# Kernel tuning notes

Measured on AMD Instinct MI355X. Metric: run time of the kernel, lower is better.

The kernel has to match this reference:

```python
import jax, jax.numpy as jnp
import numpy as np

B = 65536; D1 = 64; D2 = 64; DC = 128; K = 8; DFF = 1024
NPP = 3 * K - 1                      # 23 params per output dim (non-adaptive)
MIN_BIN = 0.1; MIN_DERIV = 1e-3; ALPHA = 2.0
DEFAULT = 3.0; DL = -DEFAULT; DD = 2 * DEFAULT; MIN_DELTA = MIN_BIN * K
SHIFT = float(np.log(np.e - 1.0))
SHIFT_DX = float(np.log(np.exp(DD - MIN_DELTA) - 1.0))
EPS = 1e-6


def setup_inputs() -> dict:
    key = jax.random.key(0)
    ks = jax.random.split(key, 8)
    x1 = jax.random.normal(ks[0], (B, D1), dtype=jnp.float32)
    x2 = jax.random.normal(ks[1], (B, D2), dtype=jnp.float32)
    context = jax.random.normal(ks[2], (B, DC), dtype=jnp.float32)
    mask1 = jnp.ones((B, D1), dtype=jnp.float32)
    din = 2 * D1 + DC
    W0 = jax.random.normal(ks[3], (din, DFF), dtype=jnp.float32) / np.sqrt(din)
    b0 = jnp.zeros((DFF,), jnp.float32)
    W1 = jax.random.normal(ks[4], (DFF, DFF), dtype=jnp.float32) / np.sqrt(DFF)
    b1 = jnp.zeros((DFF,), jnp.float32)
    W2 = jax.random.normal(ks[5], (DFF, DFF), dtype=jnp.float32) / np.sqrt(DFF)
    b2 = jnp.zeros((DFF,), jnp.float32)
    W3 = jax.random.normal(ks[6], (DFF, NPP * D2), dtype=jnp.float32) / np.sqrt(DFF)
    b3 = jnp.zeros((NPP * D2,), jnp.float32)
    return dict(x1=x1, x2=x2, context=context, mask1=mask1,
                W0=W0, b0=b0, W1=W1, b1=b1, W2=W2, b2=b2, W3=W3, b3=b3)


def _rq_forward(x1, x2, context, mask1, W0, b0, W1, b1, W2, b2, W3, b3):
    # --- conditioner MLP: input = concat(x1, mask1, context) ---
    h = jnp.concatenate([x1, mask1, context], axis=-1)
    h = jax.nn.relu(h @ W0 + b0)
    h = jax.nn.relu(h @ W1 + b1)
    h = jax.nn.relu(h @ W2 + b2)
    params = (h @ W3 + b3).reshape(x1.shape[0], D2, NPP)  # [B, D2, 23]

    w_raw = params[..., :K]
    h_raw = params[..., K:2 * K]
    d_raw = params[..., 2 * K:3 * K - 1]
    zeros = jnp.zeros(params.shape[:-1] + (1,), params.dtype)  # non-adaptive raw params

    # --- _constrain ---
    log_weight = ALPHA * jnp.tanh(zeros / ALPHA)          # -> 0
    weight = jnp.exp(log_weight)                          # -> 1
    bias = ALPHA * jnp.tanh(zeros / ALPHA)                # -> 0
    derivs = MIN_DERIV + jax.nn.softplus(d_raw + SHIFT)
    derivs = jnp.concatenate([weight, derivs, weight], axis=-1)  # [B, D2, K+1]
    left = DL + DD * jnp.tanh(zeros / DD)                 # -> -3
    delta_x = MIN_DELTA + jax.nn.softplus(zeros + SHIFT_DX)
    right = left + delta_x                                # -> +3
    bottom = weight * left + bias
    top = weight * right + bias

    w = jax.nn.softmax(w_raw, axis=-1)
    w = MIN_BIN + (1.0 - MIN_BIN * K) * w
    cw = jnp.pad(jnp.cumsum(w, axis=-1), ((0, 0), (0, 0), (1, 0)))
    cw = (right - left) * cw + left                       # cumwidths [B, D2, K+1]
    hh = jax.nn.softmax(h_raw, axis=-1)
    hh = MIN_BIN + (1.0 - MIN_BIN * K) * hh
    ch = jnp.pad(jnp.cumsum(hh, axis=-1), ((0, 0), (0, 0), (1, 0)))
    ch = (top - bottom) * ch + bottom                     # cumheights [B, D2, K+1]

    widths = cw[..., 1:] - cw[..., :-1]
    heights = ch[..., 1:] - ch[..., :-1]

    # --- bin search (searchsorted right=True on bumped cumwidths) ---
    bumped = jnp.concatenate([cw[..., :-1], cw[..., -1:] + EPS], axis=-1)
    idx = jnp.clip(jnp.sum(bumped <= x2[..., None], axis=-1) - 1, 0, K - 1)[..., None]

    gat = lambda t: jnp.take_along_axis(t, idx, axis=-1)[..., 0]
    x_k = gat(cw); x_kd = gat(widths)
    y_k = gat(ch); y_kd = gat(heights)
    s_k = gat(heights / widths)
    d0 = gat(derivs); d1 = gat(derivs[..., 1:])

    # --- forward rational-quadratic spline ---
    xi = (x2 - x_k) / x_kd
    xi1m = xi * (1.0 - xi)
    alpha_k = y_kd * (s_k * xi ** 2 + d0 * xi1m)
    beta_k = s_k + (d1 + d0 - 2.0 * s_k) * xi1m
    z_sp = y_k + alpha_k / jnp.maximum(beta_k, 1e-8)
    num = s_k ** 2 * (d1 * xi ** 2 + 2.0 * s_k * xi1m + d0 * (1.0 - xi) ** 2)
    ld_sp = jnp.log(jnp.maximum(num, 1e-8)) - 2.0 * jnp.log(jnp.maximum(beta_k, 1e-8))

    # --- affine tails ---
    lw = log_weight[..., 0]; bs = bias[..., 0]
    z_af = jnp.exp(lw) * x2 + bs
    ld_af = jnp.broadcast_to(lw, x2.shape)

    l2 = jnp.broadcast_to(left[..., 0], x2.shape)
    r2 = jnp.broadcast_to(right[..., 0], x2.shape)
    inside = (l2 <= x2) & (x2 < r2)
    z2 = jnp.where(inside, z_sp, z_af)
    ld = jnp.where(inside, ld_sp, ld_af)
    return z2, ld.sum(-1)


def reference(x1, x2, context, mask1, W0, b0, W1, b1, W2, b2, W3, b3):
    return _rq_forward(x1, x2, context, mask1, W0, b0, W1, b1, W2, b2, W3, b3)
```

## Files before the change

### kernel.cpp

```cpp
#include <hip/hip_runtime.h>


typedef __bf16 bf16_t;
typedef __bf16 bf16x8 __attribute__((ext_vector_type(8)));
typedef float f32x4 __attribute__((ext_vector_type(4)));

#define GLOAD_LDS16(g, l)                                               \
  __builtin_amdgcn_global_load_lds(                                     \
      (const __attribute__((address_space(1))) void*)(g),               \
      (__attribute__((address_space(3))) void*)(l), 16, 0, 0)

#define WAITVM(N) asm volatile("s_waitcnt vmcnt(" #N ")" ::: "memory")
#define SBAR() __builtin_amdgcn_s_barrier()

__device__ __forceinline__ void xcd_remap(int& bx, int& by) {
  const int gx = gridDim.x;
  const int nwg = gx * gridDim.y;
  const int id = blockIdx.y * gx + blockIdx.x;
  const int nid = (id & 7) * (nwg >> 3) + (id >> 3);
  bx = nid % gx;
  by = nid / gx;
}

__global__ __launch_bounds__(256) void transpose_w(
    const float* __restrict__ W, bf16_t* __restrict__ Wt,
    int K, int N, int Npad) {
  __shared__ float tile[64][65];
  const int kt = blockIdx.x * 64;
  const int nt = blockIdx.y * 64;
  const int r4 = threadIdx.x >> 6;
  const int c = threadIdx.x & 63;
#pragma unroll
  for (int i = 0; i < 16; i++) {
    int r = i * 4 + r4;
    int gn = nt + c;
    tile[r][c] = (gn < N) ? W[(size_t)(kt + r) * N + gn] : 0.0f;
  }
  __syncthreads();
#pragma unroll
  for (int i = 0; i < 16; i++) {
    int r = i * 4 + r4;
    Wt[(size_t)(nt + r) * K + kt + c] = (bf16_t)tile[c][r];
  }
}

__global__ __launch_bounds__(256) void transpose_w3p(
    const float* __restrict__ W3, bf16_t* __restrict__ Wt) {
  __shared__ float tile[64][65];
  const int kt = blockIdx.x * 64;
  const int nt = blockIdx.y * 64;
  const int r4 = threadIdx.x >> 6;
  const int c = threadIdx.x & 63;
  const int np = nt + c;
  const int d = np / 24, p = np % 24;
#pragma unroll
  for (int i = 0; i < 16; i++) {
    int r = i * 4 + r4;
    tile[r][c] = (p < 23) ? W3[(size_t)(kt + r) * 1472 + d * 23 + p] : 0.0f;
  }
  __syncthreads();
#pragma unroll
  for (int i = 0; i < 16; i++) {
    int r = i * 4 + r4;
    Wt[(size_t)(nt + r) * 1024 + kt + c] = (bf16_t)tile[c][r];
  }
}

__global__ __launch_bounds__(256) void prep_b3(const float* __restrict__ b3,
                                               float* __restrict__ b3p) {
  int t = blockIdx.x * 256 + threadIdx.x;
  if (t < 1536) {
    int d = t / 24, p = t % 24;
    b3p[t] = (p < 23) ? b3[d * 23 + p] : 0.0f;
  }
}

__global__ __launch_bounds__(256) void build_x(
    const float* __restrict__ x1, const float* __restrict__ mask1,
    const float* __restrict__ ctx, bf16_t* __restrict__ X,
    float* __restrict__ ld_out, int boff) {
  int idx = blockIdx.x * 256 + threadIdx.x;
  int bl = idx >> 8;
  int c = idx & 255;
  size_t b = (size_t)(boff + bl);
  float v;
  if (c < 64)       v = x1[b * 64 + c];
  else if (c < 128) v = mask1[b * 64 + (c - 64)];
  else              v = ctx[b * 128 + (c - 128)];
  X[(size_t)bl * 256 + c] = (bf16_t)v;
  if (c == 0) ld_out[b] = 0.0f;
}

__global__ __launch_bounds__(512, 2) void gemm_bt(
    const bf16_t* __restrict__ A, const bf16_t* __restrict__ Bt,
    const float* __restrict__ bias, bf16_t* __restrict__ Cout, int N, int K) {
  __shared__ __align__(16) bf16_t sm[65536];
  const int tid = threadIdx.x;
  const int lane = tid & 63;
  const int w = tid >> 6;
  int bx, by;
  xcd_remap(bx, by);
  const int m0 = by * 256;
  const int n0 = bx * 256;
  const int wmi = w >> 2;
  const int wnj = w & 3;
  const int lrow = lane & 15;
  const int quad = lane >> 4;

  const int byteoff = tid * 16;
  const int srow = byteoff >> 6;
  const int sqs = ((byteoff >> 4) & 3) ^ ((srow >> 1) & 3);
  const bf16_t* gA0 = A + (size_t)(m0 + srow) * K + sqs * 8;
  const bf16_t* gA1 = A + (size_t)(m0 + 128 + srow) * K + sqs * 8;
  const bf16_t* gB0 = Bt + (size_t)(n0 + srow) * K + sqs * 8;
  const bf16_t* gB1 = Bt + (size_t)(n0 + 128 + srow) * K + sqs * 8;
  const int dstT = tid * 8;

#define ST_A(PTR, D, RH)                                                 \
  do {                                                                   \
    GLOAD_LDS16(PTR, sm + (D) * 16384 + (RH) * 8192 + dstT);             \
    GLOAD_LDS16(PTR + 32, sm + (D) * 16384 + (RH) * 8192 + 4096 + dstT); \
    PTR += 64;                                                           \
  } while (0)
#define ST_B(PTR, D, CH)                                                 \
  do {                                                                   \
    GLOAD_LDS16(PTR, sm + 32768 + (D) * 16384 + (CH) * 8192 + dstT);     \
    GLOAD_LDS16(PTR + 32,                                                \
                sm + 32768 + (D) * 16384 + (CH) * 8192 + 4096 + dstT);   \
    PTR += 64;                                                           \
  } while (0)

  int aoff[8];
#pragma unroll
  for (int mi = 0; mi < 8; mi++) {
    const int r = mi * 16 + lrow;
    aoff[mi] = wmi * 8192 + r * 32 + (quad ^ ((r >> 1) & 3)) * 8;
  }
  int boff[4];
#pragma unroll
  for (int nj = 0; nj < 4; nj++) {
    const int c = (wnj & 1) * 64 + nj * 16 + lrow;
    boff[nj] = 32768 + (wnj >> 1) * 8192 + c * 32 + (quad ^ ((c >> 1) & 3)) * 8;
  }

#define RD_AF(DST, D, MIB)                                               \
  _Pragma("unroll") for (int q = 0; q < 4; q++)                          \
    _Pragma("unroll") for (int kk = 0; kk < 2; kk++)                     \
      DST[q][kk] =                                                       \
          *(const bf16x8*)(sm + (D) * 16384 + kk * 4096 + aoff[(MIB) + q]);
#define RD_BF(DST, D, NJB)                                               \
  _Pragma("unroll") for (int q = 0; q < 2; q++)                          \
    _Pragma("unroll") for (int kk = 0; kk < 2; kk++)                     \
      DST[q][kk] =                                                       \
          *(const bf16x8*)(sm + (D) * 16384 + kk * 4096 + boff[(NJB) + q]);
#define MM(AF, BF, MIB, NJB)                                             \
  __builtin_amdgcn_s_setprio(1);                                         \
  _Pragma("unroll") for (int q = 0; q < 4; q++)                          \
    _Pragma("unroll") for (int p = 0; p < 2; p++)                        \
      _Pragma("unroll") for (int kk = 0; kk < 2; kk++)                   \
        acc[(MIB) + q][(NJB) + p] = __builtin_amdgcn_mfma_f32_16x16x32_bf16( \
            AF[q][kk], BF[p][kk], acc[(MIB) + q][(NJB) + p], 0, 0, 0);   \
  __builtin_amdgcn_s_setprio(0);

  f32x4 acc[8][4];
#pragma unroll
  for (int i = 0; i < 8; i++)
#pragma unroll
    for (int j = 0; j < 4; j++) acc[i][j] = (f32x4){0.f, 0.f, 0.f, 0.f};

  ST_A(gA0, 0, 0);
  ST_A(gA1, 0, 1);
  ST_B(gB0, 0, 0);
  ST_B(gB1, 0, 1);
  ST_A(gA0, 1, 0);
  ST_A(gA1, 1, 1);

  const int nI = K >> 7;
  for (int i = 0; i < nI; i++) {
    const bool nl = (i + 1 < nI);
    bf16x8 afA[4][2], afB[4][2], bfrA[2][2], bfrB[2][2];
    WAITVM(4);
    SBAR();
    ST_B(gB0, 1, 0);
    RD_AF(afA, 0, 0);
    RD_BF(bfrA, 0, 0);
    MM(afA, bfrA, 0, 0);
    SBAR();
    ST_B(gB1, 1, 1);
    RD_AF(afB, 0, 4);
    MM(afB, bfrA, 4, 0);
    SBAR();
    if (nl) ST_A(gA0, 0, 0);
    RD_BF(bfrB, 0, 2);
    MM(afA, bfrB, 0, 2);
    SBAR();
    if (nl) ST_A(gA1, 0, 1);
    MM(afB, bfrB, 4, 2);
    if (nl) { WAITVM(4); } else { WAITVM(0); }
    SBAR();
    if (nl) ST_B(gB0, 0, 0);
    RD_AF(afA, 1, 0);
    RD_BF(bfrA, 1, 0);
    MM(afA, bfrA, 0, 0);
    SBAR();
    if (nl) ST_B(gB1, 0, 1);
    RD_AF(afB, 1, 4);
    MM(afB, bfrA, 4, 0);
    SBAR();
    if (nl) ST_A(gA0, 1, 0);
    RD_BF(bfrB, 1, 2);
    MM(afA, bfrB, 0, 2);
    SBAR();
    if (nl) ST_A(gA1, 1, 1);
    MM(afB, bfrB, 4, 2);
  }
#undef ST_A
#undef ST_B
#undef RD_AF
#undef RD_BF
#undef MM

  float bv[4];
#pragma unroll
  for (int j = 0; j < 4; j++) bv[j] = bias[n0 + wnj * 64 + j * 16 + lrow];
#pragma unroll
  for (int i = 0; i < 8; i++) {
    int rbase = m0 + wmi * 128 + i * 16 + quad * 4;
#pragma unroll
    for (int j = 0; j < 4; j++) {
      int col = n0 + wnj * 64 + j * 16 + lrow;
#pragma unroll
      for (int r = 0; r < 4; r++) {
        float v = fmaxf(acc[i][j][r] + bv[j], 0.0f);
        Cout[(size_t)(rbase + r) * N + col] = (bf16_t)v;
      }
    }
  }
}

__global__ __launch_bounds__(512, 4) void gemm_rq_fused(
    const bf16_t* __restrict__ A, const bf16_t* __restrict__ Bt,
    const float* __restrict__ b3p, const float* __restrict__ x2,
    float* __restrict__ z_out, float* __restrict__ ld_out,
    int boff, int K) {
  union alignas(16) SM {
    struct { bf16_t As[2][128 * 32]; bf16_t Bs[2][192 * 32]; } s;
    bf16_t Pt[128 * 200];
  };
  __shared__ SM sm;
  const int tid = threadIdx.x;
  const int w = tid >> 6;
  const int lane = tid & 63;
  int bx, by;
  xcd_remap(bx, by);
  const int m0 = by * 128;
  const int n0 = bx * 192;
  const int wm = (w & 1) * 64;
  const int wn = (w >> 1) * 48;
  const int lrow = lane & 15;
  const int quad = lane >> 4;

  bf16_t* const smB = &sm.s.As[0][0];

  const bf16_t* gA;
  {
    const int byteoff = (w << 10) + lane * 16;
    const int row = byteoff >> 6;
    const int qs = ((byteoff >> 4) & 3) ^ ((row >> 1) & 3);
    gA = A + (size_t)(m0 + row) * K + qs * 8;
  }
  const bf16_t* gB0;
  const bf16_t* gB1;
  {
    int byteoff = (w << 10) + lane * 16;
    int row = byteoff >> 6;
    int qs = ((byteoff >> 4) & 3) ^ ((row >> 1) & 3);
    gB0 = Bt + (size_t)(n0 + row) * K + qs * 8;
    const int c1 = (w & 3) + 8;
    byteoff = (c1 << 10) + lane * 16;
    row = byteoff >> 6;
    qs = ((byteoff >> 4) & 3) ^ ((row >> 1) & 3);
    gB1 = Bt + (size_t)(n0 + row) * K + qs * 8;
  }
  bf16_t* const dA0 = smB + w * 512;
  bf16_t* const dB0 = smB + 8192 + w * 512;
  bf16_t* const dB1 = smB + 8192 + ((w & 3) + 8) * 512;

  int offA[4], offB3[3];
#pragma unroll
  for (int i = 0; i < 4; i++) {
    const int rowA = wm + i * 16 + lrow;
    offA[i] = rowA * 32 + (quad ^ ((rowA >> 1) & 3)) * 8;
  }
#pragma unroll
  for (int j = 0; j < 3; j++) {
    const int rowB = wn + j * 16 + lrow;
    offB3[j] = rowB * 32 + (quad ^ ((rowB >> 1) & 3)) * 8;
  }

  f32x4 acc[4][3];
#pragma unroll
  for (int i = 0; i < 4; i++)
#pragma unroll
    for (int j = 0; j < 3; j++) acc[i][j] = (f32x4){0.f, 0.f, 0.f, 0.f};

  const int nPair = K >> 6;
  for (int kp = 0; kp < nPair; kp++) {
    GLOAD_LDS16(gA, dA0);
    GLOAD_LDS16(gA + 32, dA0 + 4096);
    GLOAD_LDS16(gB0, dB0);
    GLOAD_LDS16(gB0 + 32, dB0 + 6144);
    if (w < 4) {
      GLOAD_LDS16(gB1, dB1);
      GLOAD_LDS16(gB1 + 32, dB1 + 6144);
      gB1 += 64;
    }
    gA += 64;
    gB0 += 64;
    __syncthreads();
#pragma unroll
    for (int h = 0; h < 2; h++) {
      bf16x8 af[4], bfr[3];
#pragma unroll
      for (int i = 0; i < 4; i++)
        af[i] = *(const bf16x8*)(smB + h * 4096 + offA[i]);
#pragma unroll
      for (int j = 0; j < 3; j++)
        bfr[j] = *(const bf16x8*)(smB + 8192 + h * 6144 + offB3[j]);
#pragma unroll
      for (int i = 0; i < 4; i++)
#pragma unroll
        for (int j = 0; j < 3; j++)
          acc[i][j] = __builtin_amdgcn_mfma_f32_16x16x32_bf16(
              af[i], bfr[j], acc[i][j], 0, 0, 0);
    }
    __syncthreads();
  }

  float bv[3];
#pragma unroll
  for (int j = 0; j < 3; j++) bv[j] = b3p[n0 + wn + j * 16 + lrow];
#pragma unroll
  for (int i = 0; i < 4; i++) {
    const int rbase = wm + i * 16 + quad * 4;
#pragma unroll
    for (int j = 0; j < 3; j++) {
      const int col = wn + j * 16 + lrow;
#pragma unroll
      for (int r = 0; r < 4; r++)
        sm.Pt[(rbase + r) * 200 + col] = (bf16_t)(acc[i][j][r] + bv[j]);
    }
  }
  __syncthreads();

  const float SHIFT = 0.54132485f;
  const float SHIFT_DX = 5.1944682f;
  const float left = -3.0f;
  const float delta_x = 0.8f + log1pf(expf(SHIFT_DX));
  const float right = left + delta_x;
  const float scale = delta_x;
  const int dloc = tid & 7;
  const int dg = bx * 8 + dloc;

#pragma unroll
  for (int rr = 0; rr < 2; rr++) {
    const int row = (tid >> 3) + rr * 64;
    const bf16_t* pr = sm.Pt + row * 200 + dloc * 24;
    const size_t bg = (size_t)(boff + m0 + row);
    const float x = x2[bg * 64 + dg];

    bf16x8 v0 = *(const bf16x8*)(pr);
    bf16x8 v1 = *(const bf16x8*)(pr + 8);
    bf16x8 v2 = *(const bf16x8*)(pr + 16);
    float pv[24];
#pragma unroll
    for (int j = 0; j < 8; j++) pv[j] = (float)v0[j];
#pragma unroll
    for (int j = 0; j < 8; j++) pv[8 + j] = (float)v1[j];
#pragma unroll
    for (int j = 0; j < 8; j++) pv[16 + j] = (float)v2[j];

    float mw = pv[0];
#pragma unroll
    for (int j = 1; j < 8; j++) mw = fmaxf(mw, pv[j]);
    float ew[8], swv = 0.f;
#pragma unroll
    for (int j = 0; j < 8; j++) { ew[j] = expf(pv[j] - mw); swv += ew[j]; }
    float invw = 1.0f / swv;
    float cw[9];
    cw[0] = left;
    float cum = 0.f;
#pragma unroll
    for (int j = 0; j < 8; j++) {
      cum += 0.1f + 0.2f * ew[j] * invw;
      cw[j + 1] = left + scale * cum;
    }
    float mh = pv[8];
#pragma unroll
    for (int j = 9; j < 16; j++) mh = fmaxf(mh, pv[j]);
    float eh[8], shv = 0.f;
#pragma unroll
    for (int j = 0; j < 8; j++) { eh[j] = expf(pv[8 + j] - mh); shv += eh[j]; }
    float invh = 1.0f / shv;
    float chh[9];
    chh[0] = left;
    float cumh = 0.f;
#pragma unroll
    for (int j = 0; j < 8; j++) {
      cumh += 0.1f + 0.2f * eh[j] * invh;
      chh[j + 1] = left + scale * cumh;
    }
    float dv[9];
    dv[0] = 1.0f;
    dv[8] = 1.0f;
#pragma unroll
    for (int j = 0; j < 7; j++) {
      float v = pv[16 + j] + SHIFT;
      dv[j + 1] = 0.001f + ((v > 20.f) ? v : log1pf(expf(v)));
    }
    int cnt = 0;
#pragma unroll
    for (int j = 0; j < 8; j++) cnt += (cw[j] <= x) ? 1 : 0;
    cnt += ((cw[8] + 1e-6f) <= x) ? 1 : 0;
    int idx = cnt - 1;
    idx = idx < 0 ? 0 : (idx > 7 ? 7 : idx);
    float x_k = cw[0], x_k1 = cw[1], y_k = chh[0], y_k1 = chh[1];
    float d0v = dv[0], d1v = dv[1];
#pragma unroll
    for (int j = 1; j < 8; j++) {
      bool s = (idx == j);
      x_k = s ? cw[j] : x_k;
      x_k1 = s ? cw[j + 1] : x_k1;
      y_k = s ? chh[j] : y_k;
      y_k1 = s ? chh[j + 1] : y_k1;
      d0v = s ? dv[j] : d0v;
      d1v = s ? dv[j + 1] : d1v;
    }
    float x_kd = x_k1 - x_k;
    float y_kd = y_k1 - y_k;
    float s_k = y_kd / x_kd;
    float xi = (x - x_k) / x_kd;
    float xi1m = xi * (1.f - xi);
    float alpha_k = y_kd * (s_k * xi * xi + d0v * xi1m);
    float beta_k = s_k + (d1v + d0v - 2.f * s_k) * xi1m;
    float z_sp = y_k + alpha_k / fmaxf(beta_k, 1e-8f);
    float oxi = 1.f - xi;
    float num = s_k * s_k * (d1v * xi * xi + 2.f * s_k * xi1m + d0v * oxi * oxi);
    float ld_sp = logf(fmaxf(num, 1e-8f)) - 2.f * logf(fmaxf(beta_k, 1e-8f));

    bool inside = (left <= x) && (x < right);
    z_out[bg * 64 + dg] = inside ? z_sp : x;
    float ldv = inside ? ld_sp : 0.f;
    ldv += __shfl_xor(ldv, 1);
    ldv += __shfl_xor(ldv, 2);
    ldv += __shfl_xor(ldv, 4);
    if (dloc == 0) atomicAdd(&ld_out[bg], ldv);
  }
}

extern "C" void kernel_launch(void* const* d_in, const int* in_sizes, int n_in,
                              void* d_out, int out_size, void* d_ws,
                              size_t ws_size, hipStream_t stream) {
  const float* x1 = (const float*)d_in[0];
  const float* x2 = (const float*)d_in[1];
  const float* ctx = (const float*)d_in[2];
  const float* mask1 = (const float*)d_in[3];
  const float* W0 = (const float*)d_in[4];
  const float* b0 = (const float*)d_in[5];
  const float* W1 = (const float*)d_in[6];
  const float* b1 = (const float*)d_in[7];
  const float* W2 = (const float*)d_in[8];
  const float* b2 = (const float*)d_in[9];
  const float* W3 = (const float*)d_in[10];
  const float* b3 = (const float*)d_in[11];
  float* out = (float*)d_out;

  const int B = 65536;
  char* ws = (char*)d_ws;

  bf16_t* Wt0 = (bf16_t*)ws;
  bf16_t* Wt1 = (bf16_t*)(ws + 524288);
  bf16_t* Wt2 = (bf16_t*)(ws + 524288 + 2097152);
  bf16_t* Wt3 = (bf16_t*)(ws + 524288 + 2 * 2097152);
  float* b3p = (float*)(ws + 524288 + 2 * 2097152 + 3145728);
  const size_t wend = 524288 + 2 * 2097152 + 3145728 + 8192;

  int C = 4;
  if (wend + (size_t)B * 4096 <= ws_size) C = 1;
  else if (wend + (size_t)(B / 2) * 4096 <= ws_size) C = 2;
  const int Bc = B / C;
  bf16_t* HA = (bf16_t*)(ws + wend);
  char* R = ws + wend + (size_t)Bc * 2048;
  bf16_t* X = (bf16_t*)R;
  bf16_t* HB = (bf16_t*)R;
  float* ld_out = out + (size_t)B * 64;

  transpose_w<<<dim3(4, 16), 256, 0, stream>>>(W0, Wt0, 256, 1024, 1024);
  transpose_w<<<dim3(16, 16), 256, 0, stream>>>(W1, Wt1, 1024, 1024, 1024);
  transpose_w<<<dim3(16, 16), 256, 0, stream>>>(W2, Wt2, 1024, 1024, 1024);
  transpose_w3p<<<dim3(16, 24), 256, 0, stream>>>(W3, Wt3);
  prep_b3<<<6, 256, 0, stream>>>(b3, b3p);

  for (int c = 0; c < C; c++) {
    const int boff = c * Bc;
    build_x<<<Bc, 256, 0, stream>>>(x1, mask1, ctx, X, ld_out, boff);
    gemm_bt<<<dim3(4, Bc / 256), 512, 0, stream>>>(X, Wt0, b0, HA, 1024, 256);
    gemm_bt<<<dim3(4, Bc / 256), 512, 0, stream>>>(HA, Wt1, b1, HB, 1024, 1024);
    gemm_bt<<<dim3(4, Bc / 256), 512, 0, stream>>>(HB, Wt2, b2, HA, 1024, 1024);
    gemm_rq_fused<<<dim3(8, Bc / 128), 512, 0, stream>>>(
        HA, Wt3, b3p, x2, out, ld_out, boff, 1024);
  }
}
```

Baseline: 758.0 us.

## Retile final fused GEMM to 256-row pipelined tiles and merge prep kernels

The final GEMM+spline kernel moves from 128x192 tiles with a simple load-sync-compute loop to 256x192 tiles. It uses a double-buffered, interleaved global-to-LDS schedule with partial vmcnt waits, barriers and MFMA priority hints, so loads overlap compute and each B tile is reused across more rows. Occupancy drops from 4 to 2 blocks per CU. Separately, the weight transposes, bias packing and input build are merged into one launch to cut launch overhead.

```diff
diff --git a/kernel.cpp b/kernel.cpp
--- a/kernel.cpp
+++ b/kernel.cpp
@@ -22,73 +22,72 @@
   by = nid / gx;
 }
 
-__global__ __launch_bounds__(256) void transpose_w(
-    const float* __restrict__ W, bf16_t* __restrict__ Wt,
-    int K, int N, int Npad) {
+__global__ __launch_bounds__(256) void prep_all(
+    const float* __restrict__ x1, const float* __restrict__ mask1,
+    const float* __restrict__ ctx, const float* __restrict__ W0,
+    const float* __restrict__ W1, const float* __restrict__ W2,
+    const float* __restrict__ W3, const float* __restrict__ b3,
+    bf16_t* __restrict__ X, float* __restrict__ ld_out,
+    bf16_t* __restrict__ Wt0, bf16_t* __restrict__ Wt1,
+    bf16_t* __restrict__ Wt2, bf16_t* __restrict__ Wt3,
+    float* __restrict__ b3p, int boff, int Bc) {
   __shared__ float tile[64][65];
-  const int kt = blockIdx.x * 64;
-  const int nt = blockIdx.y * 64;
-  const int r4 = threadIdx.x >> 6;
-  const int c = threadIdx.x & 63;
-#pragma unroll
-  for (int i = 0; i < 16; i++) {
-    int r = i * 4 + r4;
-    int gn = nt + c;
-    tile[r][c] = (gn < N) ? W[(size_t)(kt + r) * N + gn] : 0.0f;
-  }
-  __syncthreads();
-#pragma unroll
-  for (int i = 0; i < 16; i++) {
-    int r = i * 4 + r4;
-    Wt[(size_t)(nt + r) * K + kt + c] = (bf16_t)tile[c][r];
-  }
-}
-
-__global__ __launch_bounds__(256) void transpose_w3p(
-    const float* __restrict__ W3, bf16_t* __restrict__ Wt) {
-  __shared__ float tile[64][65];
-  const int kt = blockIdx.x * 64;
-  const int nt = blockIdx.y * 64;
-  const int r4 = threadIdx.x >> 6;
-  const int c = threadIdx.x & 63;
-  const int np = nt + c;
-  const int d = np / 24, p = np % 24;
-#pragma unroll
-  for (int i = 0; i < 16; i++) {
-    int r = i * 4 + r4;
-    tile[r][c] = (p < 23) ? W3[(size_t)(kt + r) * 1472 + d * 23 + p] : 0.0f;
-  }
-  __syncthreads();
-#pragma unroll
-  for (int i = 0; i < 16; i++) {
-    int r = i * 4 + r4;
-    Wt[(size_t)(nt + r) * 1024 + kt + c] = (bf16_t)tile[c][r];
-  }
-}
-
-__global__ __launch_bounds__(256) void prep_b3(const float* __restrict__ b3,
-                                               float* __restrict__ b3p) {
-  int t = blockIdx.x * 256 + threadIdx.x;
-  if (t < 1536) {
-    int d = t / 24, p = t % 24;
-    b3p[t] = (p < 23) ? b3[d * 23 + p] : 0.0f;
-  }
-}
-
-__global__ __launch_bounds__(256) void build_x(
-    const float* __restrict__ x1, const float* __restrict__ mask1,
-    const float* __restrict__ ctx, bf16_t* __restrict__ X,
-    float* __restrict__ ld_out, int boff) {
-  int idx = blockIdx.x * 256 + threadIdx.x;
-  int bl = idx >> 8;
-  int c = idx & 255;
-  size_t b = (size_t)(boff + bl);
-  float v;
-  if (c < 64)       v = x1[b * 64 + c];
-  else if (c < 128) v = mask1[b * 64 + (c - 64)];
-  else              v = ctx[b * 128 + (c - 128)];
-  X[(size_t)bl * 256 + c] = (bf16_t)v;
-  if (c == 0) ld_out[b] = 0.0f;
+  const int tid = threadIdx.x;
+  int id = blockIdx.x;
+  if (id < Bc) {
+    const int c = tid;
+    const size_t b = (size_t)(boff + id);
+    float v;
+    if (c < 64)       v = x1[b * 64 + c];
+    else if (c < 128) v = mask1[b * 64 + (c - 64)];
+    else              v = ctx[b * 128 + (c - 128)];
+    X[(size_t)id * 256 + c] = (bf16_t)v;
+    if (c == 0) ld_out[b] = 0.0f;
+    return;
+  }
+  id -= Bc;
+  const int r4 = tid >> 6;
+  const int cc = tid & 63;
+  const float* W = nullptr;
+  bf16_t* Wt = nullptr;
+  int K = 0, N = 0, kt = 0, nt = 0;
+  bool w3 = false;
+  if (id < 64)       { W = W0; Wt = Wt0; K = 256;  N = 1024; kt = (id & 3) * 64;  nt = (id >> 2) * 64; }
+  else if (id < 320) { int j = id - 64;  W = W1; Wt = Wt1; K = 1024; N = 1024; kt = (j & 15) * 64; nt = (j >> 4) * 64; }
+  else if (id < 576) { int j = id - 320; W = W2; Wt = Wt2; K = 1024; N = 1024; kt = (j & 15) * 64; nt = (j >> 4) * 64; }
+  else if (id < 960) { int j = id - 576; K = 1024; kt = (j & 15) * 64; nt = (j >> 4) * 64; w3 = true; }
+  else {
+    int t = (id - 960) * 256 + tid;
+    if (t < 1536) { int d = t / 24, p = t % 24; b3p[t] = (p < 23) ? b3[d * 23 + p] : 0.0f; }
+    return;
+  }
+  if (!w3) {
+#pragma unroll
+    for (int i = 0; i < 16; i++) {
+      int r = i * 4 + r4;
+      int gn = nt + cc;
+      tile[r][cc] = (gn < N) ? W[(size_t)(kt + r) * N + gn] : 0.0f;
+    }
+    __syncthreads();
+#pragma unroll
+    for (int i = 0; i < 16; i++) {
+      int r = i * 4 + r4;
+      Wt[(size_t)(nt + r) * K + kt + cc] = (bf16_t)tile[cc][r];
+    }
+  } else {
+    const int np = nt + cc, d = np / 24, p = np % 24;
+#pragma unroll
+    for (int i = 0; i < 16; i++) {
+      int r = i * 4 + r4;
+      tile[r][cc] = (p < 23) ? W3[(size_t)(kt + r) * 1472 + d * 23 + p] : 0.0f;
+    }
+    __syncthreads();
+#pragma unroll
+    for (int i = 0; i < 16; i++) {
+      int r = i * 4 + r4;
+      Wt3[(size_t)(nt + r) * 1024 + kt + cc] = (bf16_t)tile[cc][r];
+    }
+  }
 }
 
 __global__ __launch_bounds__(512, 2) void gemm_bt(
@@ -238,117 +237,169 @@
   }
 }
 
-__global__ __launch_bounds__(512, 4) void gemm_rq_fused(
+__global__ __launch_bounds__(512, 2) void gemm_rq_fused(
     const bf16_t* __restrict__ A, const bf16_t* __restrict__ Bt,
     const float* __restrict__ b3p, const float* __restrict__ x2,
     float* __restrict__ z_out, float* __restrict__ ld_out,
     int boff, int K) {
-  union alignas(16) SM {
-    struct { bf16_t As[2][128 * 32]; bf16_t Bs[2][192 * 32]; } s;
-    bf16_t Pt[128 * 200];
-  };
-  __shared__ SM sm;
+  __shared__ __align__(16) bf16_t sm[57344];
   const int tid = threadIdx.x;
+  const int lane = tid & 63;
   const int w = tid >> 6;
-  const int lane = tid & 63;
   int bx, by;
   xcd_remap(bx, by);
-  const int m0 = by * 128;
+  const int m0 = by * 256;
   const int n0 = bx * 192;
-  const int wm = (w & 1) * 64;
-  const int wn = (w >> 1) * 48;
+  const int wmi = w >> 2;
+  const int wnj = w & 3;
   const int lrow = lane & 15;
   const int quad = lane >> 4;
 
-  bf16_t* const smB = &sm.s.As[0][0];
-
-  const bf16_t* gA;
-  {
-    const int byteoff = (w << 10) + lane * 16;
-    const int row = byteoff >> 6;
-    const int qs = ((byteoff >> 4) & 3) ^ ((row >> 1) & 3);
-    gA = A + (size_t)(m0 + row) * K + qs * 8;
-  }
-  const bf16_t* gB0;
-  const bf16_t* gB1;
-  {
-    int byteoff = (w << 10) + lane * 16;
-    int row = byteoff >> 6;
-    int qs = ((byteoff >> 4) & 3) ^ ((row >> 1) & 3);
-    gB0 = Bt + (size_t)(n0 + row) * K + qs * 8;
-    const int c1 = (w & 3) + 8;
-    byteoff = (c1 << 10) + lane * 16;
-    row = byteoff >> 6;
-    qs = ((byteoff >> 4) & 3) ^ ((row >> 1) & 3);
-    gB1 = Bt + (size_t)(n0 + row) * K + qs * 8;
-  }
-  bf16_t* const dA0 = smB + w * 512;
-  bf16_t* const dB0 = smB + 8192 + w * 512;
-  bf16_t* const dB1 = smB + 8192 + ((w & 3) + 8) * 512;
-
-  int offA[4], offB3[3];
-#pragma unroll
-  for (int i = 0; i < 4; i++) {
-    const int rowA = wm + i * 16 + lrow;
-    offA[i] = rowA * 32 + (quad ^ ((rowA >> 1) & 3)) * 8;
-  }
-#pragma unroll
-  for (int j = 0; j < 3; j++) {
-    const int rowB = wn + j * 16 + lrow;
-    offB3[j] = rowB * 32 + (quad ^ ((rowB >> 1) & 3)) * 8;
-  }
-
-  f32x4 acc[4][3];
-#pragma unroll
-  for (int i = 0; i < 4; i++)
+  const int byteoff = tid * 16;
+  const int srow = byteoff >> 6;
+  const int sqs = ((byteoff >> 4) & 3) ^ ((srow >> 1) & 3);
+  const bf16_t* gA0 = A + (size_t)(m0 + srow) * K + sqs * 8;
+  const bf16_t* gA1 = A + (size_t)(m0 + 128 + srow) * K + sqs * 8;
+  const int scol = tid >> 3;
+  const int sdc = (tid & 7) ^ (scol & 7);
+  const bf16_t* gB0c = Bt + (size_t)(n0 + scol) * K + sdc * 8;
+  const bf16_t* gB1c = Bt + (size_t)(n0 + 64 + scol) * K + sdc * 8;
+  const bf16_t* gB2c = Bt + (size_t)(n0 + 128 + scol) * K + sdc * 8;
+  const int dstT = tid * 8;
+
+#define FST_A(PTR, D, RH)                                                \
+  do {                                                                   \
+    GLOAD_LDS16(PTR, sm + (D) * 16384 + (RH) * 8192 + dstT);             \
+    GLOAD_LDS16(PTR + 32, sm + (D) * 16384 + (RH) * 8192 + 4096 + dstT); \
+    PTR += 64;                                                           \
+  } while (0)
+#define FST_B(PTR, D, CH)                                                \
+  do {                                                                   \
+    GLOAD_LDS16(PTR, sm + 32768 + (D) * 12288 + (CH) * 4096 + dstT);     \
+    PTR += 64;                                                           \
+  } while (0)
+
+  int aoff[8];
+#pragma unroll
+  for (int mi = 0; mi < 8; mi++) {
+    const int r = mi * 16 + lrow;
+    aoff[mi] = wmi * 8192 + r * 32 + (quad ^ ((r >> 1) & 3)) * 8;
+  }
+  int boffs[3][2];
+#pragma unroll
+  for (int nj = 0; nj < 3; nj++) {
+#pragma unroll
+    for (int kk = 0; kk < 2; kk++) {
+      const int c = wnj * 48 + nj * 16 + lrow;
+      const int ch = c >> 6, ccol = c & 63;
+      boffs[nj][kk] =
+          32768 + ch * 4096 + ccol * 64 + ((((kk << 2) | quad)) ^ (ccol & 7)) * 8;
+    }
+  }
+
+#define FRD_A(DST, D, MIB)                                               \
+  _Pragma("unroll") for (int q = 0; q < 4; q++)                          \
+    _Pragma("unroll") for (int kk = 0; kk < 2; kk++)                     \
+      DST[q][kk] =                                                       \
+          *(const bf16x8*)(sm + (D) * 16384 + kk * 4096 + aoff[(MIB) + q]);
+#define FRD_B01(D)                                                       \
+  _Pragma("unroll") for (int nj = 0; nj < 2; nj++)                       \
+    _Pragma("unroll") for (int kk = 0; kk < 2; kk++)                     \
+      bfr[nj][kk] = *(const bf16x8*)(sm + (D) * 12288 + boffs[nj][kk]);
+#define FRD_B2(D)                                                        \
+  _Pragma("unroll") for (int kk = 0; kk < 2; kk++)                       \
+    bfr[2][kk] = *(const bf16x8*)(sm + (D) * 12288 + boffs[2][kk]);
+#define FMM16(AF, MIB)                                                   \
+  __builtin_amdgcn_s_setprio(1);                                         \
+  _Pragma("unroll") for (int q = 0; q < 4; q++)                          \
+    _Pragma("unroll") for (int p = 0; p < 2; p++)                        \
+      _Pragma("unroll") for (int kk = 0; kk < 2; kk++)                   \
+        acc[(MIB) + q][p] = __builtin_amdgcn_mfma_f32_16x16x32_bf16(     \
+            AF[q][kk], bfr[p][kk], acc[(MIB) + q][p], 0, 0, 0);          \
+  __builtin_amdgcn_s_setprio(0);
+#define FMM8(AF, MIB)                                                    \
+  __builtin_amdgcn_s_setprio(1);                                         \
+  _Pragma("unroll") for (int q = 0; q < 4; q++)                          \
+    _Pragma("unroll") for (int kk = 0; kk < 2; kk++)                     \
+      acc[(MIB) + q][2] = __builtin_amdgcn_mfma_f32_16x16x32_bf16(       \
+          AF[q][kk], bfr[2][kk], acc[(MIB) + q][2], 0, 0, 0);            \
+  __builtin_amdgcn_s_setprio(0);
+
+  f32x4 acc[8][3];
+#pragma unroll
+  for (int i = 0; i < 8; i++)
 #pragma unroll
     for (int j = 0; j < 3; j++) acc[i][j] = (f32x4){0.f, 0.f, 0.f, 0.f};
 
-  const int nPair = K >> 6;
-  for (int kp = 0; kp < nPair; kp++) {
-    GLOAD_LDS16(gA, dA0);
-    GLOAD_LDS16(gA + 32, dA0 + 4096);
-    GLOAD_LDS16(gB0, dB0);
-    GLOAD_LDS16(gB0 + 32, dB0 + 6144);
-    if (w < 4) {
-      GLOAD_LDS16(gB1, dB1);
-      GLOAD_LDS16(gB1 + 32, dB1 + 6144);
-      gB1 += 64;
-    }
-    gA += 64;
-    gB0 += 64;
-    __syncthreads();
-#pragma unroll
-    for (int h = 0; h < 2; h++) {
-      bf16x8 af[4], bfr[3];
-#pragma unroll
-      for (int i = 0; i < 4; i++)
-        af[i] = *(const bf16x8*)(smB + h * 4096 + offA[i]);
-#pragma unroll
-      for (int j = 0; j < 3; j++)
-        bfr[j] = *(const bf16x8*)(smB + 8192 + h * 6144 + offB3[j]);
-#pragma unroll
-      for (int i = 0; i < 4; i++)
-#pragma unroll
-        for (int j = 0; j < 3; j++)
-          acc[i][j] = __builtin_amdgcn_mfma_f32_16x16x32_bf16(
-              af[i], bfr[j], acc[i][j], 0, 0, 0);
-    }
-    __syncthreads();
-  }
+  FST_A(gA0, 0, 0);
+  FST_A(gA1, 0, 1);
+  FST_B(gB0c, 0, 0);
+  FST_B(gB1c, 0, 1);
+  FST_B(gB2c, 0, 2);
+  FST_A(gA0, 1, 0);
+  FST_A(gA1, 1, 1);
+
+  const int nI = K >> 7;
+  for (int i = 0; i < nI; i++) {
+    const bool nl = (i + 1 < nI);
+    bf16x8 afA[4][2], afB[4][2], bfr[3][2];
+    WAITVM(4);
+    SBAR();
+    FST_B(gB0c, 1, 0);
+    FST_B(gB1c, 1, 1);
+    FRD_A(afA, 0, 0);
+    FRD_B01(0);
+    FMM16(afA, 0);
+    SBAR();
+    FST_B(gB2c, 1, 2);
+    FRD_A(afB, 0, 4);
+    FMM16(afB, 4);
+    SBAR();
+    if (nl) FST_A(gA0, 0, 0);
+    FRD_B2(0);
+    FMM8(afA, 0);
+    SBAR();
+    if (nl) FST_A(gA1, 0, 1);
+    FMM8(afB, 4);
+    if (nl) { WAITVM(4); } else { WAITVM(0); }
+    SBAR();
+    if (nl) { FST_B(gB0c, 0, 0); FST_B(gB1c, 0, 1); }
+    FRD_A(afA, 1, 0);
+    FRD_B01(1);
+    FMM16(afA, 0);
+    SBAR();
+    if (nl) FST_B(gB2c, 0, 2);
+    FRD_A(afB, 1, 4);
+    FMM16(afB, 4);
+    SBAR();
+    if (nl) FST_A(gA0, 1, 0);
+    FRD_B2(1);
+    FMM8(afA, 0);
+    SBAR();
+    if (nl) FST_A(gA1, 1, 1);
+    FMM8(afB, 4);
+  }
+#undef FST_A
+#undef FST_B
+#undef FRD_A
+#undef FRD_B01
+#undef FRD_B2
+#undef FMM16
+#undef FMM8
+  __syncthreads();
 
   float bv[3];
 #pragma unroll
-  for (int j = 0; j < 3; j++) bv[j] = b3p[n0 + wn + j * 16 + lrow];
-#pragma unroll
-  for (int i = 0; i < 4; i++) {
-    const int rbase = wm + i * 16 + quad * 4;
+  for (int j = 0; j < 3; j++) bv[j] = b3p[n0 + wnj * 48 + j * 16 + lrow];
+#pragma unroll
+  for (int i = 0; i < 8; i++) {
+    const int rbase = wmi * 128 + i * 16 + quad * 4;
 #pragma unroll
     for (int j = 0; j < 3; j++) {
-      const int col = wn + j * 16 + lrow;
+      const int col = wnj * 48 + j * 16 + lrow;
 #pragma unroll
       for (int r = 0; r < 4; r++)
-        sm.Pt[(rbase + r) * 200 + col] = (bf16_t)(acc[i][j][r] + bv[j]);
+        sm[(rbase + r) * 200 + col] = (bf16_t)(acc[i][j][r] + bv[j]);
     }
   }
   __syncthreads();
@@ -363,9 +414,9 @@
   const int dg = bx * 8 + dloc;
 
 #pragma unroll
-  for (int rr = 0; rr < 2; rr++) {
+  for (int rr = 0; rr < 4; rr++) {
     const int row = (tid >> 3) + rr * 64;
-    const bf16_t* pr = sm.Pt + row * 200 + dloc * 24;
+    const bf16_t* pr = sm + row * 200 + dloc * 24;
     const size_t bg = (size_t)(boff + m0 + row);
     const float x = x2[bg * 64 + dg];
 
@@ -495,19 +546,15 @@
   bf16_t* HB = (bf16_t*)R;
   float* ld_out = out + (size_t)B * 64;
 
-  transpose_w<<<dim3(4, 16), 256, 0, stream>>>(W0, Wt0, 256, 1024, 1024);
-  transpose_w<<<dim3(16, 16), 256, 0, stream>>>(W1, Wt1, 1024, 1024, 1024);
-  transpose_w<<<dim3(16, 16), 256, 0, stream>>>(W2, Wt2, 1024, 1024, 1024);
-  transpose_w3p<<<dim3(16, 24), 256, 0, stream>>>(W3, Wt3);
-  prep_b3<<<6, 256, 0, stream>>>(b3, b3p);
-
   for (int c = 0; c < C; c++) {
     const int boff = c * Bc;
-    build_x<<<Bc, 256, 0, stream>>>(x1, mask1, ctx, X, ld_out, boff);
+    prep_all<<<Bc + (c == 0 ? 966 : 0), 256, 0, stream>>>(
+        x1, mask1, ctx, W0, W1, W2, W3, b3, X, ld_out,
+        Wt0, Wt1, Wt2, Wt3, b3p, boff, Bc);
     gemm_bt<<<dim3(4, Bc / 256), 512, 0, stream>>>(X, Wt0, b0, HA, 1024, 256);
     gemm_bt<<<dim3(4, Bc / 256), 512, 0, stream>>>(HA, Wt1, b1, HB, 1024, 1024);
     gemm_bt<<<dim3(4, Bc / 256), 512, 0, stream>>>(HB, Wt2, b2, HA, 1024, 1024);
-    gemm_rq_fused<<<dim3(8, Bc / 128), 512, 0, stream>>>(
+    gemm_rq_fused<<<dim3(8, Bc / 256), 512, 0, stream>>>(
         HA, Wt3, b3p, x2, out, ld_out, boff, 1024);
   }
 }
```

Result: slower. 776.4 us (+2.4%).
